# Kernel tuning notes

Hardware: AMD Instinct MI355X
Metric: run time of the kernel (lower is better)

## Reference

```python
import jax, jax.numpy as jnp
import numpy as np

def mish(x):
    return x * jnp.tanh(jax.nn.softplus(x))

def setup_inputs() -> dict:
    ANT, RF, DS, G, B = 64, 8, 8, 16, 4096
    BB_DIM = 2 * RF * DS      # 128
    RF_DIM = 2 * ANT * RF     # 1024
    key = jax.random.key(0)
    ks = jax.random.split(key, 10)
    def lin(kw, kb, i, o):
        lim = 1.0 / np.sqrt(i)
        W = jax.random.uniform(kw, (o, i), jnp.float32, -lim, lim)
        b = jax.random.uniform(kb, (o,), jnp.float32, -lim, lim)
        return W, b
    W_rfbb, b_rfbb = lin(ks[0], ks[1], RF_DIM, BB_DIM)
    W_rfrf, b_rfrf = lin(ks[2], ks[3], RF_DIM, RF_DIM)
    W_bbrf, b_bbrf = lin(ks[4], ks[5], BB_DIM, RF_DIM)
    W_bbbb, b_bbbb = lin(ks[6], ks[7], BB_DIM, BB_DIM)
    BB_feature = jax.random.normal(ks[8], (B, G, BB_DIM), jnp.float32)
    RF_feature = jax.random.normal(ks[9], (B, RF_DIM), jnp.float32)
    return {
        "BB_feature": BB_feature, "RF_feature": RF_feature,
        "W_rfbb": W_rfbb, "b_rfbb": b_rfbb,
        "W_rfrf": W_rfrf, "b_rfrf": b_rfrf,
        "W_bbrf": W_bbrf, "b_bbrf": b_bbrf,
        "W_bbbb": W_bbbb, "b_bbbb": b_bbbb,
    }

def reference(BB_feature, RF_feature, W_rfbb, b_rfbb, W_rfrf, b_rfrf, W_bbrf, b_bbrf, W_bbbb, b_bbbb):
    # mean over subcarrier-group dim
    BB_mean = jnp.mean(BB_feature, axis=-2)                      # [B, BB_DIM]
    RF_to_RF = mish(RF_feature @ W_rfrf.T + b_rfrf)              # [B, RF_DIM]
    RF_to_BB = mish(RF_feature @ W_rfbb.T + b_rfbb)              # [B, BB_DIM]
    BB_to_RF = mish(BB_mean @ W_bbrf.T + b_bbrf)                 # [B, RF_DIM]
    BB_to_BB = mish(jnp.einsum('bgi,oi->bgo', BB_feature, W_bbbb) + b_bbbb)  # [B, G, BB_DIM]
    new_RF = RF_to_RF + BB_to_RF
    new_BB = BB_to_BB + RF_to_BB[:, None, :]
    return (new_BB, new_RF)
```

## Files before the change

kernel.cpp:

```cpp
#include <hip/hip_runtime.h>
#include <hip/hip_bf16.h>

typedef __attribute__((ext_vector_type(8))) short short8;
typedef __attribute__((ext_vector_type(4))) short short4v;
typedef __attribute__((ext_vector_type(4))) float floatx4;

#define BDIM 128
#define RDIM 1024
#define NB   4096
#define NG   16
#define LDP  40

__device__ __forceinline__ float mishf(float x) {
    float e = __expf(x);
    float t = e * (e + 2.0f);
    float r = x * (t / (t + 2.0f));
    return x > 20.0f ? x : r;
}

__device__ __forceinline__ short8 cvt8v(float4 f0, float4 f1) {
    union { __hip_bfloat162 h; unsigned u; } c0, c1, c2, c3;
    c0.h = __float22bfloat162_rn(make_float2(f0.x, f0.y));
    c1.h = __float22bfloat162_rn(make_float2(f0.z, f0.w));
    c2.h = __float22bfloat162_rn(make_float2(f1.x, f1.y));
    c3.h = __float22bfloat162_rn(make_float2(f1.z, f1.w));
    union { short8 s; unsigned u[4]; } r;
    r.u[0] = c0.u; r.u[1] = c1.u; r.u[2] = c2.u; r.u[3] = c3.u;
    return r.s;
}

__device__ __forceinline__ short4v cvt4v(float4 f) {
    union { __hip_bfloat162 h; unsigned u; } c0, c1;
    c0.h = __float22bfloat162_rn(make_float2(f.x, f.y));
    c1.h = __float22bfloat162_rn(make_float2(f.z, f.w));
    union { short4v s; unsigned u[2]; } r;
    r.u[0] = c0.u; r.u[1] = c1.u;
    return r.s;
}

__device__ __forceinline__ void gld16(const void* g, void* l) {
    __builtin_amdgcn_global_load_lds(
        (const __attribute__((address_space(1))) unsigned int*)g,
        (__attribute__((address_space(3))) unsigned int*)l, 16, 0, 0);
}

#define MFMA(a, b, c) __builtin_amdgcn_mfma_f32_16x16x32_bf16(a, b, c, 0, 0, 0)

#define C1       4194304u
#define C2       5242880u
#define C3       5373952u
#define C4       5505024u
#define CT       5521408u
#define FLATB    1536

__global__ void __launch_bounds__(256) k_prep(
    const float* __restrict__ bb, const float* __restrict__ rf,
    const float* __restrict__ Wrfrf, const float* __restrict__ Wrfbb,
    const float* __restrict__ Wbbrf, const float* __restrict__ Wbbbb,
    short* __restrict__ bb_b, short* __restrict__ mean_b, short* __restrict__ rf_b,
    short* __restrict__ wrfrf_b, short* __restrict__ wrfbb_b,
    short* __restrict__ wbbrf_b, short* __restrict__ wbbbb_b)
{
    int bid = blockIdx.x;
    int tid = threadIdx.x;
    if (bid < 512) {
        int b = bid * 8 + (tid >> 5);
        int d = (tid & 31) * 4;
        const float4* p = (const float4*)(bb + (size_t)b * (NG * BDIM) + d);
        short* ob = bb_b + (size_t)b * (NG * BDIM) + d;
        float4 s = {0.f, 0.f, 0.f, 0.f};
        #pragma unroll
        for (int g = 0; g < NG; ++g) {
            float4 v = p[g * (BDIM / 4)];
            s.x += v.x; s.y += v.y; s.z += v.z; s.w += v.w;
            *(short4v*)(ob + g * BDIM) = cvt4v(v);
        }
        s.x *= 0.0625f; s.y *= 0.0625f; s.z *= 0.0625f; s.w *= 0.0625f;
        *(short4v*)(mean_b + (size_t)b * BDIM + d) = cvt4v(s);
    } else {
        size_t t = (size_t)(bid - 512) * 256 + tid;
        for (size_t base = t * 8; base < CT; base += (size_t)FLATB * 256 * 8) {
            const float* s; short* dst; size_t off;
            if (base < C1)      { s = rf;    dst = rf_b;    off = base; }
            else if (base < C2) { s = Wrfrf; dst = wrfrf_b; off = base - C1; }
            else if (base < C3) { s = Wrfbb; dst = wrfbb_b; off = base - C2; }
            else if (base < C4) { s = Wbbrf; dst = wbbrf_b; off = base - C3; }
            else                { s = Wbbbb; dst = wbbbb_b; off = base - C4; }
            float4 f0 = ((const float4*)(s + off))[0];
            float4 f1 = ((const float4*)(s + off))[1];
            *(short8*)(dst + off) = cvt8v(f0, f1);
        }
    }
}

__global__ void __launch_bounds__(256) k_newrf(
    const short* __restrict__ rfb,
    const short* __restrict__ meanb,
    const short* __restrict__ wrfrfb,
    const float* __restrict__ brfrf,
    const short* __restrict__ wbbrfb,
    const float* __restrict__ bbbrf,
    const short* __restrict__ wrfbbb,
    const float* __restrict__ brfbb,
    float* __restrict__ out,
    float* __restrict__ rf2bb)
{
    __shared__ short As[2][128 * LDP];
    __shared__ short Bs[2][64 * LDP];
    __shared__ short Ws2[2][16 * LDP];
    int tid = threadIdx.x;
    int wave = tid >> 6, lane = tid & 63;
    int r = lane & 15, quad = lane >> 4;
    int wm = (wave & 1) * 64, wn = (wave >> 1) * 32;
    int mt = blockIdx.x >> 4, nt = blockIdx.x & 15;
    int m0 = mt * 128, n0 = nt * 64;
    bool doP = (nt < 8);

    int arow = tid >> 1, akh = (tid & 1) * 16;
    int brow = tid >> 2, bkq = (tid & 3) * 8;
    int aidx = arow * LDP + akh;
    int bidx = brow * LDP + bkq;
    int widx = (tid >> 2) * LDP + bkq;

    const short* aG = rfb    + (size_t)(m0 + arow) * RDIM + akh;
    const short* bG = wrfrfb + (size_t)(n0 + brow) * RDIM + bkq;
    const short* wG = wrfbbb + (size_t)(nt * 16 + (tid >> 2)) * RDIM + bkq;

    floatx4 acc1[4][2], acc2[4][2], acc3[4];
    #pragma unroll
    for (int mi = 0; mi < 4; ++mi) {
        acc1[mi][0] = floatx4{0.f,0.f,0.f,0.f}; acc1[mi][1] = acc1[mi][0];
        acc2[mi][0] = acc1[mi][0]; acc2[mi][1] = acc1[mi][0];
        acc3[mi] = acc1[mi][0];
    }
    short8 ra0, ra1, rb0, rw0;
    bool wload = doP && (tid < 64);

    ra0 = ((const short8*)aG)[0]; ra1 = ((const short8*)aG)[1];
    rb0 = ((const short8*)bG)[0];
    if (wload) rw0 = ((const short8*)wG)[0];
    *(short8*)&As[0][aidx]     = ra0;
    *(short8*)&As[0][aidx + 8] = ra1;
    *(short8*)&Bs[0][bidx]     = rb0;
    if (wload) *(short8*)&Ws2[0][widx] = rw0;
    ra0 = ((const short8*)(aG + 32))[0]; ra1 = ((const short8*)(aG + 32))[1];
    rb0 = ((const short8*)(bG + 32))[0];
    if (wload) rw0 = ((const short8*)(wG + 32))[0];
    __syncthreads();

    for (int it = 0; it < 32; ++it) {
        const short* Ac = As[it & 1];
        const short* Bc = Bs[it & 1];
        const short* Wc = Ws2[it & 1];
        short8 af[4];
        #pragma unroll
        for (int mi = 0; mi < 4; ++mi)
            af[mi] = *(const short8*)&Ac[(wm + mi * 16 + r) * LDP + quad * 8];
        short8 bf[2];
        bf[0] = *(const short8*)&Bc[(wn + r) * LDP + quad * 8];
        bf[1] = *(const short8*)&Bc[(wn + 16 + r) * LDP + quad * 8];
        #pragma unroll
        for (int mi = 0; mi < 4; ++mi) {
            acc1[mi][0] = MFMA(af[mi], bf[0], acc1[mi][0]);
            acc1[mi][1] = MFMA(af[mi], bf[1], acc1[mi][1]);
        }
        if (doP && (wave & 2) == 0) {
            short8 b2 = *(const short8*)&Wc[r * LDP + quad * 8];
            #pragma unroll
            for (int mi = 0; mi < 4; ++mi) acc3[mi] = MFMA(af[mi], b2, acc3[mi]);
        }
        if (it < 31) {
            int nb = (it + 1) & 1;
            *(short8*)&As[nb][aidx]     = ra0;
            *(short8*)&As[nb][aidx + 8] = ra1;
            *(short8*)&Bs[nb][bidx]     = rb0;
            if (wload) *(short8*)&Ws2[nb][widx] = rw0;
        }
        if (it < 30) {
            int k = (it + 2) * 32;
            ra0 = ((const short8*)(aG + k))[0]; ra1 = ((const short8*)(aG + k))[1];
            rb0 = ((const short8*)(bG + k))[0];
            if (wload) rw0 = ((const short8*)(wG + k))[0];
        }
        __syncthreads();
    }

    const short* a2G = meanb  + (size_t)(m0 + arow) * BDIM + akh;
    const short* b2G = wbbrfb + (size_t)(n0 + brow) * BDIM + bkq;
    ra0 = ((const short8*)a2G)[0]; ra1 = ((const short8*)a2G)[1];
    rb0 = ((const short8*)b2G)[0];
    *(short8*)&As[0][aidx]     = ra0;
    *(short8*)&As[0][aidx + 8] = ra1;
    *(short8*)&Bs[0][bidx]     = rb0;
    ra0 = ((const short8*)(a2G + 32))[0]; ra1 = ((const short8*)(a2G + 32))[1];
    rb0 = ((const short8*)(b2G + 32))[0];
    __syncthreads();
    for (int it = 0; it < 4; ++it) {
        const short* Ac = As[it & 1];
        const short* Bc = Bs[it & 1];
        short8 af[4];
        #pragma unroll
        for (int mi = 0; mi < 4; ++mi)
            af[mi] = *(const short8*)&Ac[(wm + mi * 16 + r) * LDP + quad * 8];
        short8 bf[2];
        bf[0] = *(const short8*)&Bc[(wn + r) * LDP + quad * 8];
        bf[1] = *(const short8*)&Bc[(wn + 16 + r) * LDP + quad * 8];
        #pragma unroll
        for (int mi = 0; mi < 4; ++mi) {
            acc2[mi][0] = MFMA(af[mi], bf[0], acc2[mi][0]);
            acc2[mi][1] = MFMA(af[mi], bf[1], acc2[mi][1]);
        }
        if (it < 3) {
            int nb = (it + 1) & 1;
            *(short8*)&As[nb][aidx]     = ra0;
            *(short8*)&As[nb][aidx + 8] = ra1;
            *(short8*)&Bs[nb][bidx]     = rb0;
        }
        if (it < 2) {
            int k = (it + 2) * 32;
            ra0 = ((const short8*)(a2G + k))[0]; ra1 = ((const short8*)(a2G + k))[1];
            rb0 = ((const short8*)(b2G + k))[0];
        }
        __syncthreads();
    }

    #pragma unroll
    for (int nj = 0; nj < 2; ++nj) {
        int col = n0 + wn + nj * 16 + r;
        float b1 = brfrf[col];
        float b2 = bbbrf[col];
        #pragma unroll
        for (int mi = 0; mi < 4; ++mi) {
            #pragma unroll
            for (int g = 0; g < 4; ++g) {
                int row = m0 + wm + mi * 16 + quad * 4 + g;
                out[(size_t)row * RDIM + col] =
                    mishf(acc1[mi][nj][g] + b1) + mishf(acc2[mi][nj][g] + b2);
            }
        }
    }
    if (doP && (wave & 2) == 0) {
        int col = nt * 16 + r;
        float bs = brfbb[col];
        #pragma unroll
        for (int mi = 0; mi < 4; ++mi) {
            #pragma unroll
            for (int g = 0; g < 4; ++g) {
                int row = m0 + wm + mi * 16 + quad * 4 + g;
                rf2bb[(size_t)row * BDIM + col] = mishf(acc3[mi][g] + bs);
            }
        }
    }
}

__global__ void __launch_bounds__(256) k_newbb(
    const short* __restrict__ bbb,
    const short* __restrict__ wb,
    const float* __restrict__ bias,
    const float* __restrict__ rf2bb,
    float* __restrict__ out)
{
    __shared__ alignas(16) short At[64 * 128];
    __shared__ alignas(16) short Wt[128 * 128];
    int tid = threadIdx.x;
    int wave = tid >> 6, lane = tid & 63;
    int r = lane & 15, quad = lane >> 4;
    size_t m0 = (size_t)blockIdx.x * 64;

    int lrow = lane >> 4;
    int lslot = lane & 15;
    #pragma unroll
    for (int j = 0; j < 8; ++j) {
        int row = wave * 32 + j * 4 + lrow;
        int col = ((lslot ^ (row & 7)) << 3);
        gld16(wb + (size_t)row * BDIM + col, &Wt[(wave * 32 + j * 4) * 128]);
    }
    #pragma unroll
    for (int j = 0; j < 4; ++j) {
        int row = wave * 16 + j * 4 + lrow;
        int col = ((lslot ^ (row & 7)) << 3);
        gld16(bbb + (m0 + row) * BDIM + col, &At[(wave * 16 + j * 4) * 128]);
    }

    floatx4 acc[8];
    #pragma unroll
    for (int j = 0; j < 8; ++j) acc[j] = floatx4{0.f,0.f,0.f,0.f};

    size_t prow = (m0 >> 4) + wave;

    __syncthreads();

    #pragma unroll
    for (int kc = 0; kc < 4; ++kc) {
        int sw = (((kc << 2) + quad) ^ (r & 7)) << 3;
        short8 a = *(const short8*)&At[(wave * 16 + r) * 128 + sw];
        #pragma unroll
        for (int nj = 0; nj < 8; ++nj) {
            short8 b = *(const short8*)&Wt[(nj * 16 + r) * 128 + sw];
            acc[nj] = MFMA(a, b, acc[nj]);
        }
    }

    #pragma unroll
    for (int nj = 0; nj < 8; ++nj) {
        int col = nj * 16 + r;
        float bs = bias[col];
        float pv = rf2bb[prow * BDIM + col];
        #pragma unroll
        for (int g = 0; g < 4; ++g) {
            size_t row = m0 + wave * 16 + quad * 4 + g;
            out[row * BDIM + col] = mishf(acc[nj][g] + bs) + pv;
        }
    }
}

extern "C" void kernel_launch(void* const* d_in, const int* in_sizes, int n_in,
                              void* d_out, int out_size, void* d_ws, size_t ws_size,
                              hipStream_t stream) {
    const float* BB    = (const float*)d_in[0];
    const float* RF    = (const float*)d_in[1];
    const float* Wrfbb = (const float*)d_in[2];
    const float* brfbb = (const float*)d_in[3];
    const float* Wrfrf = (const float*)d_in[4];
    const float* brfrf = (const float*)d_in[5];
    const float* Wbbrf = (const float*)d_in[6];
    const float* bbbrf = (const float*)d_in[7];
    const float* Wbbbb = (const float*)d_in[8];
    const float* bbbbb = (const float*)d_in[9];

    float* outBB = (float*)d_out;
    float* outRF = outBB + (size_t)NB * NG * BDIM;

    char* w = (char*)d_ws;
    short* mean_b  = (short*)(w);
    short* rf_b    = (short*)(w + 1048576);
    short* wrfrf_b = (short*)(w + 9437184);
    short* wrfbb_b = (short*)(w + 11534336);
    short* wbbrf_b = (short*)(w + 11796480);
    short* wbbbb_b = (short*)(w + 12058624);
    short* bb_b    = (short*)(w + 12091392);
    float* rf2bb   = (float*)(w + 28868608);

    k_prep <<<512 + FLATB, 256, 0, stream>>>(BB, RF, Wrfrf, Wrfbb, Wbbrf, Wbbbb,
                                             bb_b, mean_b, rf_b, wrfrf_b, wrfbb_b,
                                             wbbrf_b, wbbbb_b);
    k_newrf<<<512, 256, 0, stream>>>(rf_b, mean_b, wrfrf_b, brfrf, wbbrf_b, bbbrf,
                                     wrfbb_b, brfbb, outRF, rf2bb);
    k_newbb<<<1024, 256, 0, stream>>>(bb_b, wbbbb_b, bbbbb, rf2bb, outBB);
}
```

Measured before the change: 154.2 us.

## Split RF GEMM into 64x64 tiles with separate RF-to-BB tiles and XCD swizzle

The RF kernel now uses 64x64 output tiles instead of 128x64, and the RF_to_BB projection becomes its own set of tile blocks (two extra column tiles per row block) instead of extra MFMAs piggybacked onto some blocks. The grid grows from 512 to 1152 blocks, and the block index is remapped across 8 groups, likely for XCD locality. The first load of the mean-feature GEMM is prefetched during the last main-loop iteration. This targets the load imbalance from the extra P work and the low occupancy of a 512-block grid, at the cost of less data reuse per tile.

```diff
diff --git a/kernel.cpp b/kernel.cpp
--- a/kernel.cpp
+++ b/kernel.cpp
@@ -105,149 +105,119 @@
     float* __restrict__ out,
     float* __restrict__ rf2bb)
 {
-    __shared__ short As[2][128 * LDP];
+    __shared__ short As[2][64 * LDP];
     __shared__ short Bs[2][64 * LDP];
-    __shared__ short Ws2[2][16 * LDP];
     int tid = threadIdx.x;
     int wave = tid >> 6, lane = tid & 63;
     int r = lane & 15, quad = lane >> 4;
-    int wm = (wave & 1) * 64, wn = (wave >> 1) * 32;
-    int mt = blockIdx.x >> 4, nt = blockIdx.x & 15;
-    int m0 = mt * 128, n0 = nt * 64;
-    bool doP = (nt < 8);
-
-    int arow = tid >> 1, akh = (tid & 1) * 16;
-    int brow = tid >> 2, bkq = (tid & 3) * 8;
-    int aidx = arow * LDP + akh;
-    int bidx = brow * LDP + bkq;
-    int widx = (tid >> 2) * LDP + bkq;
-
-    const short* aG = rfb    + (size_t)(m0 + arow) * RDIM + akh;
-    const short* bG = wrfrfb + (size_t)(n0 + brow) * RDIM + bkq;
-    const short* wG = wrfbbb + (size_t)(nt * 16 + (tid >> 2)) * RDIM + bkq;
-
-    floatx4 acc1[4][2], acc2[4][2], acc3[4];
-    #pragma unroll
-    for (int mi = 0; mi < 4; ++mi) {
+    int wm = (wave & 1) * 32, wn = (wave >> 1) * 32;
+    int bid = (blockIdx.x & 7) * 144 + (blockIdx.x >> 3);
+    int mt = bid / 18, nt = bid % 18;
+    int m0 = mt * 64;
+    bool isP = (nt >= 16);
+    const short* Bsrc = isP ? (wrfbbb + (size_t)(nt - 16) * 64 * RDIM)
+                            : (wrfrfb + (size_t)nt * 64 * RDIM);
+
+    int srow = tid >> 2, skq = (tid & 3) * 8;
+    int sidx = srow * LDP + skq;
+    const short* aG  = rfb  + (size_t)(m0 + srow) * RDIM + skq;
+    const short* bG  = Bsrc + (size_t)srow * RDIM + skq;
+    const short* a2G = meanb + (size_t)(m0 + srow) * BDIM + skq;
+    const short* b2G = wbbrfb + (size_t)(nt * 64 + srow) * BDIM + skq;
+
+    floatx4 acc1[2][2], acc2[2][2];
+    #pragma unroll
+    for (int mi = 0; mi < 2; ++mi) {
         acc1[mi][0] = floatx4{0.f,0.f,0.f,0.f}; acc1[mi][1] = acc1[mi][0];
         acc2[mi][0] = acc1[mi][0]; acc2[mi][1] = acc1[mi][0];
-        acc3[mi] = acc1[mi][0];
-    }
-    short8 ra0, ra1, rb0, rw0;
-    bool wload = doP && (tid < 64);
-
-    ra0 = ((const short8*)aG)[0]; ra1 = ((const short8*)aG)[1];
-    rb0 = ((const short8*)bG)[0];
-    if (wload) rw0 = ((const short8*)wG)[0];
-    *(short8*)&As[0][aidx]     = ra0;
-    *(short8*)&As[0][aidx + 8] = ra1;
-    *(short8*)&Bs[0][bidx]     = rb0;
-    if (wload) *(short8*)&Ws2[0][widx] = rw0;
-    ra0 = ((const short8*)(aG + 32))[0]; ra1 = ((const short8*)(aG + 32))[1];
-    rb0 = ((const short8*)(bG + 32))[0];
-    if (wload) rw0 = ((const short8*)(wG + 32))[0];
+    }
+
+    short8 ra, rb;
+    ra = *(const short8*)aG; rb = *(const short8*)bG;
+    *(short8*)&As[0][sidx] = ra; *(short8*)&Bs[0][sidx] = rb;
+    ra = *(const short8*)(aG + 32); rb = *(const short8*)(bG + 32);
     __syncthreads();
 
     for (int it = 0; it < 32; ++it) {
         const short* Ac = As[it & 1];
         const short* Bc = Bs[it & 1];
-        const short* Wc = Ws2[it & 1];
-        short8 af[4];
-        #pragma unroll
-        for (int mi = 0; mi < 4; ++mi)
-            af[mi] = *(const short8*)&Ac[(wm + mi * 16 + r) * LDP + quad * 8];
-        short8 bf[2];
+        short8 af[2], bf[2];
+        af[0] = *(const short8*)&Ac[(wm + r) * LDP + quad * 8];
+        af[1] = *(const short8*)&Ac[(wm + 16 + r) * LDP + quad * 8];
         bf[0] = *(const short8*)&Bc[(wn + r) * LDP + quad * 8];
         bf[1] = *(const short8*)&Bc[(wn + 16 + r) * LDP + quad * 8];
-        #pragma unroll
-        for (int mi = 0; mi < 4; ++mi) {
-            acc1[mi][0] = MFMA(af[mi], bf[0], acc1[mi][0]);
-            acc1[mi][1] = MFMA(af[mi], bf[1], acc1[mi][1]);
-        }
-        if (doP && (wave & 2) == 0) {
-            short8 b2 = *(const short8*)&Wc[r * LDP + quad * 8];
-            #pragma unroll
-            for (int mi = 0; mi < 4; ++mi) acc3[mi] = MFMA(af[mi], b2, acc3[mi]);
-        }
+        acc1[0][0] = MFMA(af[0], bf[0], acc1[0][0]);
+        acc1[0][1] = MFMA(af[0], bf[1], acc1[0][1]);
+        acc1[1][0] = MFMA(af[1], bf[0], acc1[1][0]);
+        acc1[1][1] = MFMA(af[1], bf[1], acc1[1][1]);
         if (it < 31) {
             int nb = (it + 1) & 1;
-            *(short8*)&As[nb][aidx]     = ra0;
-            *(short8*)&As[nb][aidx + 8] = ra1;
-            *(short8*)&Bs[nb][bidx]     = rb0;
-            if (wload) *(short8*)&Ws2[nb][widx] = rw0;
+            *(short8*)&As[nb][sidx] = ra;
+            *(short8*)&Bs[nb][sidx] = rb;
         }
         if (it < 30) {
             int k = (it + 2) * 32;
-            ra0 = ((const short8*)(aG + k))[0]; ra1 = ((const short8*)(aG + k))[1];
-            rb0 = ((const short8*)(bG + k))[0];
-            if (wload) rw0 = ((const short8*)(wG + k))[0];
+            ra = *(const short8*)(aG + k); rb = *(const short8*)(bG + k);
+        } else if (it == 30 && !isP) {
+            ra = *(const short8*)a2G; rb = *(const short8*)b2G;
         }
         __syncthreads();
     }
 
-    const short* a2G = meanb  + (size_t)(m0 + arow) * BDIM + akh;
-    const short* b2G = wbbrfb + (size_t)(n0 + brow) * BDIM + bkq;
-    ra0 = ((const short8*)a2G)[0]; ra1 = ((const short8*)a2G)[1];
-    rb0 = ((const short8*)b2G)[0];
-    *(short8*)&As[0][aidx]     = ra0;
-    *(short8*)&As[0][aidx + 8] = ra1;
-    *(short8*)&Bs[0][bidx]     = rb0;
-    ra0 = ((const short8*)(a2G + 32))[0]; ra1 = ((const short8*)(a2G + 32))[1];
-    rb0 = ((const short8*)(b2G + 32))[0];
-    __syncthreads();
-    for (int it = 0; it < 4; ++it) {
-        const short* Ac = As[it & 1];
-        const short* Bc = Bs[it & 1];
-        short8 af[4];
-        #pragma unroll
-        for (int mi = 0; mi < 4; ++mi)
-            af[mi] = *(const short8*)&Ac[(wm + mi * 16 + r) * LDP + quad * 8];
-        short8 bf[2];
-        bf[0] = *(const short8*)&Bc[(wn + r) * LDP + quad * 8];
-        bf[1] = *(const short8*)&Bc[(wn + 16 + r) * LDP + quad * 8];
-        #pragma unroll
-        for (int mi = 0; mi < 4; ++mi) {
-            acc2[mi][0] = MFMA(af[mi], bf[0], acc2[mi][0]);
-            acc2[mi][1] = MFMA(af[mi], bf[1], acc2[mi][1]);
-        }
-        if (it < 3) {
-            int nb = (it + 1) & 1;
-            *(short8*)&As[nb][aidx]     = ra0;
-            *(short8*)&As[nb][aidx + 8] = ra1;
-            *(short8*)&Bs[nb][bidx]     = rb0;
-        }
-        if (it < 2) {
-            int k = (it + 2) * 32;
-            ra0 = ((const short8*)(a2G + k))[0]; ra1 = ((const short8*)(a2G + k))[1];
-            rb0 = ((const short8*)(b2G + k))[0];
-        }
+    if (!isP) {
+        *(short8*)&As[0][sidx] = ra; *(short8*)&Bs[0][sidx] = rb;
+        ra = *(const short8*)(a2G + 32); rb = *(const short8*)(b2G + 32);
         __syncthreads();
-    }
-
-    #pragma unroll
-    for (int nj = 0; nj < 2; ++nj) {
-        int col = n0 + wn + nj * 16 + r;
-        float b1 = brfrf[col];
-        float b2 = bbbrf[col];
-        #pragma unroll
-        for (int mi = 0; mi < 4; ++mi) {
+        for (int it = 0; it < 4; ++it) {
+            const short* Ac = As[it & 1];
+            const short* Bc = Bs[it & 1];
+            short8 af[2], bf[2];
+            af[0] = *(const short8*)&Ac[(wm + r) * LDP + quad * 8];
+            af[1] = *(const short8*)&Ac[(wm + 16 + r) * LDP + quad * 8];
+            bf[0] = *(const short8*)&Bc[(wn + r) * LDP + quad * 8];
+            bf[1] = *(const short8*)&Bc[(wn + 16 + r) * LDP + quad * 8];
+            acc2[0][0] = MFMA(af[0], bf[0], acc2[0][0]);
+            acc2[0][1] = MFMA(af[0], bf[1], acc2[0][1]);
+            acc2[1][0] = MFMA(af[1], bf[0], acc2[1][0]);
+            acc2[1][1] = MFMA(af[1], bf[1], acc2[1][1]);
+            if (it < 3) {
+                int nb = (it + 1) & 1;
+                *(short8*)&As[nb][sidx] = ra;
+                *(short8*)&Bs[nb][sidx] = rb;
+            }
+            if (it < 2) {
+                int k = (it + 2) * 32;
+                ra = *(const short8*)(a2G + k); rb = *(const short8*)(b2G + k);
+            }
+            __syncthreads();
+        }
+        #pragma unroll
+        for (int nj = 0; nj < 2; ++nj) {
+            int col = nt * 64 + wn + nj * 16 + r;
+            float b1 = brfrf[col];
+            float b2 = bbbrf[col];
             #pragma unroll
-            for (int g = 0; g < 4; ++g) {
-                int row = m0 + wm + mi * 16 + quad * 4 + g;
-                out[(size_t)row * RDIM + col] =
-                    mishf(acc1[mi][nj][g] + b1) + mishf(acc2[mi][nj][g] + b2);
+            for (int mi = 0; mi < 2; ++mi) {
+                #pragma unroll
+                for (int g = 0; g < 4; ++g) {
+                    int row = m0 + wm + mi * 16 + quad * 4 + g;
+                    out[(size_t)row * RDIM + col] =
+                        mishf(acc1[mi][nj][g] + b1) + mishf(acc2[mi][nj][g] + b2);
+                }
             }
         }
-    }
-    if (doP && (wave & 2) == 0) {
-        int col = nt * 16 + r;
-        float bs = brfbb[col];
-        #pragma unroll
-        for (int mi = 0; mi < 4; ++mi) {
+    } else {
+        #pragma unroll
+        for (int nj = 0; nj < 2; ++nj) {
+            int colL = (nt - 16) * 64 + wn + nj * 16 + r;
+            float bs = brfbb[colL];
             #pragma unroll
-            for (int g = 0; g < 4; ++g) {
-                int row = m0 + wm + mi * 16 + quad * 4 + g;
-                rf2bb[(size_t)row * BDIM + col] = mishf(acc3[mi][g] + bs);
+            for (int mi = 0; mi < 2; ++mi) {
+                #pragma unroll
+                for (int g = 0; g < 4; ++g) {
+                    int row = m0 + wm + mi * 16 + quad * 4 + g;
+                    rf2bb[(size_t)row * BDIM + colL] = mishf(acc1[mi][nj][g] + bs);
+                }
             }
         }
     }
@@ -344,7 +314,7 @@
     k_prep <<<512 + FLATB, 256, 0, stream>>>(BB, RF, Wrfrf, Wrfbb, Wbbrf, Wbbbb,
                                              bb_b, mean_b, rf_b, wrfrf_b, wrfbb_b,
                                              wbbrf_b, wbbbb_b);
-    k_newrf<<<512, 256, 0, stream>>>(rf_b, mean_b, wrfrf_b, brfrf, wbbrf_b, bbbrf,
-                                     wrfbb_b, brfbb, outRF, rf2bb);
+    k_newrf<<<1152, 256, 0, stream>>>(rf_b, mean_b, wrfrf_b, brfrf, wbbrf_b, bbbrf,
+                                      wrfbb_b, brfbb, outRF, rf2bb);
     k_newbb<<<1024, 256, 0, stream>>>(bb_b, wbbbb_b, bbbbb, rf2bb, outBB);
 }
```

Measured after the change: 154.4 us. About the same (+0.2%).
